# Optimization experiments

Hardware: AMD Instinct MI355X
Metric: run time of the kernel (lower is better)

## Reference

```python
import jax, jax.numpy as jnp
import numpy as np

M = 8      # bits // 8 experts
SUB = 8    # sub-code width per expert
HID = 256  # expert output classes (2**SUB)
BITS = 64
NCLS = 100
NUM_FLIP = (BITS // 32) ** 2  # 4


def _bit_flip(x, template, key):
    # torch: rand.argsort(-1) -> shuffledTemplate = template[idx]; x[mask] *= -1
    rand = jax.random.uniform(key, x.shape)
    idx = jnp.argsort(rand, axis=-1)
    mask = template[idx]
    return jnp.where(mask, -x, x)


def _map_net(x, W1, b1, W2, b2):
    # m independent Linear(8,256)->SiLU->Linear(256,256) experts over contiguous chunks
    N = x.shape[0]
    xs = x.reshape(N, M, SUB)
    h = jax.nn.silu(jnp.einsum('nmi,mih->nmh', xs, W1) + b1)
    return jnp.einsum('nmh,mho->nmo', h, W2) + b2  # [N, M, HID]


def setup_inputs() -> dict:
    key = jax.random.key(0)
    ks = jax.random.split(key, 10)
    N = 32768
    x = jax.random.normal(ks[0], (N, BITS), jnp.float32)
    # multi-label targets, guarantee >=1 positive per row (meanWeight divides by row sum)
    y = (jax.random.uniform(ks[1], (N, NCLS)) < 0.1).astype(jnp.int32)
    lab = jax.random.randint(ks[2], (N,), 0, NCLS)
    y = y.at[jnp.arange(N), lab].set(1)
    centroids = (jax.random.uniform(ks[3], (NCLS, BITS)) > 0.5).astype(jnp.float32)
    permIdx = jax.random.permutation(ks[4], BITS)

    def make_template(k):
        t = jnp.zeros(BITS, bool).at[:NUM_FLIP].set(True)
        return jax.random.permutation(k, t)

    template_map = make_template(ks[5])
    template_raw = make_template(ks[6])
    W1 = jax.random.normal(ks[7], (M, SUB, HID), jnp.float32) / np.sqrt(SUB)
    b1 = jnp.zeros((M, HID), jnp.float32)
    W2 = jax.random.normal(ks[8], (M, HID, HID), jnp.float32) / np.sqrt(HID)
    b2 = jnp.zeros((M, HID), jnp.float32)
    return dict(x=x, y=y, centroids=centroids, permIdx=permIdx,
                template_map=template_map, template_raw=template_raw,
                W1=W1, b1=b1, W2=W2, b2=b2)


def reference(x, y, centroids, permIdx, template_map, template_raw, W1, b1, W2, b2):
    N = x.shape[0]
    multiplier = 2 ** jnp.arange(SUB)  # [8]
    kmap, kraw = jax.random.split(jax.random.key(1))

    xp = x[:, permIdx]  # permuted codes [N, BITS]
    x_det = jax.lax.stop_gradient(xp)

    # ---- mapLoss path (x detached; mapper params still trained; dropout in eval) ----
    logits_map = _map_net(_bit_flip(x_det, template_map, kmap), W1, b1, W2, b2)  # [N,M,HID]
    raw_flipped = _bit_flip(x_det, template_raw, kraw)
    binary = raw_flipped.reshape(N, M, SUB) > 0
    target = (binary * multiplier).sum(-1)  # [N, M] decimal sub-codes
    lse = jax.nn.logsumexp(logits_map, axis=-1)
    picked = jnp.take_along_axis(logits_map, target[..., None], axis=-1)[..., 0]
    mapLoss = (lse - picked).mean(0).sum()  # sum over m of per-chunk CE means
    hitRate = (logits_map.argmax(-1) == target).astype(jnp.float32).mean()

    # ---- netLoss path (mapper on non-detached x, no flip; centers detached) ----
    hashCenter = jax.lax.stop_gradient(centroids[:, permIdx])  # [C, BITS]
    centerBits = hashCenter > 0
    centerTarget = (centerBits.reshape(NCLS, M, SUB) * multiplier).sum(-1)  # [C, M]
    logits_net = _map_net(xp, W1, b1, W2, b2)  # [N, M, HID]
    lse2 = jax.nn.logsumexp(logits_net, axis=-1)  # [N, M]
    # picked2[n,m,c] = logits_net[n, m, centerTarget[c, m]]
    picked2 = logits_net[:, jnp.arange(M)[:, None], centerTarget.T]  # [N, M, C]
    ce = lse2[..., None] - picked2  # [N, M, C]
    mask = y > 0
    w = mask.astype(jnp.float32)
    w = w / w.sum(-1, keepdims=True)  # meanWeight (mask * meanWeight == meanWeight)
    netLoss = (ce * w[:, None, :]).sum() / N

    # ---- codes-to-center Hamming distance, masked mean over (n, c) with y>0 ----
    xb = (xp > 0).astype(jnp.float32)
    cb = centerBits.astype(jnp.float32)
    ham = xb.sum(-1, keepdims=True) + cb.sum(-1)[None, :] - 2.0 * (xb @ cb.T)  # [N, C]
    mf = mask.astype(jnp.float32)
    codesToCenterDistance = (ham * mf).sum() / mf.sum()

    total = netLoss + mapLoss
    return (total, netLoss, mapLoss, hitRate, codesToCenterDistance)
```

## Files before the change

kernel.cpp:

```cpp
#include <hip/hip_runtime.h>
#include <stdint.h>

#define NR 32768
#define MM 8
#define NCLS 100
#define HALFN 1048576u
#define HSS 260
#define LGS 260
#define PSS 12

#define LOG2E 1.4426950408889634f
#define LN2F  0.6931471805599453f

typedef _Float16 h8 __attribute__((ext_vector_type(8)));
typedef _Float16 h4 __attribute__((ext_vector_type(4)));
typedef float f4 __attribute__((ext_vector_type(4)));
typedef unsigned long long ull;

__host__ __device__ inline void tf2x32(uint32_t k0, uint32_t k1, uint32_t x0, uint32_t x1,
                                       uint32_t& o0, uint32_t& o1) {
  uint32_t ks0 = k0, ks1 = k1, ks2 = k0 ^ k1 ^ 0x1BD11BDAu;
  x0 += ks0; x1 += ks1;
#define TFR(r) { x0 += x1; x1 = (x1 << r) | (x1 >> (32 - r)); x1 ^= x0; }
  TFR(13) TFR(15) TFR(26) TFR(6)  x0 += ks1; x1 += ks2 + 1u;
  TFR(17) TFR(29) TFR(16) TFR(24) x0 += ks2; x1 += ks0 + 2u;
  TFR(13) TFR(15) TFR(26) TFR(6)  x0 += ks0; x1 += ks1 + 3u;
  TFR(17) TFR(29) TFR(16) TFR(24) x0 += ks1; x1 += ks2 + 4u;
  TFR(13) TFR(15) TFR(26) TFR(6)  x0 += ks2; x1 += ks0 + 5u;
#undef TFR
  o0 = x0; o1 = x1;
}

__device__ inline int load_tmpl(const void* p, int lane) {
  const unsigned* pi = (const unsigned*)p;
  unsigned w = pi[lane];
  ull okF = __ballot(w == 0u || w == 0x3F800000u);
  ull onF = __ballot(w == 0x3F800000u);
  ull okI = __ballot(w <= 1u);
  ull onI = __ballot(w == 1u);
  if (okF == ~0ull && __popcll(onF) == 4) return (w == 0x3F800000u) ? 1 : 0;
  if (okI == ~0ull && __popcll(onI) == 4) return (int)w;
  const unsigned char* pb = (const unsigned char*)p;
  return pb[lane] ? 1 : 0;
}

__device__ inline uint32_t packh2(float a, float b) {
  union { _Float16 h[2]; uint32_t u; } cv;
  cv.h[0] = (_Float16)a; cv.h[1] = (_Float16)b;
  return cv.u;
}

__device__ inline ull flip_mask(ull tmask, uint32_t key) {
  ull fm = 0;
  while (tmask) {
    int p = __ffsll((long long)tmask) - 1;
    tmask &= tmask - 1;
    uint32_t kp = (uint32_t)__builtin_amdgcn_readlane((int)key, p);
    fm |= 1ull << __popcll(__ballot(key < kp));
  }
  return fm;
}

__global__ __launch_bounds__(256) void stage1p(
    const float* __restrict__ x, const int* __restrict__ y, const int* __restrict__ perm,
    const void* tmap, const void* traw,
    uint32_t km0, uint32_t km1, uint32_t kr0, uint32_t kr1,
    const float* __restrict__ W2, const float* __restrict__ W1,
    const float* __restrict__ B1, const float* __restrict__ B2,
    const float* __restrict__ centroids,
    _Float16* __restrict__ Wp, _Float16* __restrict__ Wp1, float* __restrict__ B2s,
    ull* __restrict__ cb64,
    uint32_t* __restrict__ xp16, uint32_t* __restrict__ xm16,
    ull* __restrict__ targ, ull* __restrict__ xb,
    float* __restrict__ winv, unsigned char* __restrict__ poslist, int* __restrict__ nposA) {
  int b = blockIdx.x, tid = threadIdx.x;
  if (b >= NR / 4) {
    int pb = b - NR / 4;
    if (pb < 256) {
      int gid = pb * 256 + tid;
      int lane6 = gid & 63, frag = gid >> 6;
      int NT = frag & 15, kt = (frag >> 4) & 7, m = frag >> 7;
      int q = lane6 >> 4, lr = lane6 & 15;
      const float* src = W2 + (size_t)m * 65536 + (size_t)(kt * 32 + q * 8) * 256 + NT * 16 + lr;
      h8 v;
#pragma unroll
      for (int j = 0; j < 8; j++) v[j] = (_Float16)src[j * 256];
      *(h8*)(Wp + (size_t)gid * 8) = v;
    } else if (pb < 288) {
      int idx = (pb - 256) * 256 + tid;
      int lane = idx & 63, t = (idx >> 6) & 15, m = idx >> 10;
      int q = lane >> 4, lr = lane & 15;
      h8 v;
#pragma unroll
      for (int j = 0; j < 8; j++) {
        float val = 0.0f;
        if (q == 0) val = W1[(size_t)(m * 8 + j) * 256 + t * 16 + lr] * LOG2E;
        else if (q == 1 && j == 0) val = B1[m * 256 + t * 16 + lr] * LOG2E;
        v[j] = (_Float16)val;
      }
      *(h8*)(Wp1 + (size_t)idx * 8) = v;
    } else if (pb < 313) {
      int c = (pb - 288) * 4 + (tid >> 6);
      int lane = tid & 63;
      ull bits = __ballot(centroids[c * 64 + perm[lane]] > 0.0f);
      if (lane == 0 && c < NCLS) cb64[c] = bits;
    } else {
#pragma unroll
      for (int j = 0; j < 8; j++) B2s[tid * 8 + j] = B2[tid * 8 + j] * LOG2E;
    }
    return;
  }

  __shared__ uint32_t ex[8][64];
  int wv = tid >> 6, lane = tid & 63;
  int odd = wv & 1, hi = wv >> 1;
  int n = b * 2 + odd + hi * 16384;

  int tm = load_tmpl(tmap, lane);
  int tr = load_tmpl(traw, lane);
  float xpv = x[n * 64 + perm[lane]];

  {
    uint32_t ic = (uint32_t)((b * 2 + hi) * 64 + lane);
    uint32_t k0 = odd ? kr0 : km0, k1 = odd ? kr1 : km1;
    uint32_t o0, o1;
    tf2x32(k0, k1, ic, ic + HALFN, o0, o1);
    ex[hi * 4 + odd * 2 + 0][lane] = o0;
    ex[hi * 4 + odd * 2 + 1][lane] = o1;
  }
  __syncthreads();
  uint32_t bm = ex[odd * 4 + 0 * 2 + hi][lane];
  uint32_t br = ex[odd * 4 + 1 * 2 + hi][lane];

  uint32_t kmk = ((bm >> 9) << 6) | (uint32_t)lane;
  uint32_t krk = ((br >> 9) << 6) | (uint32_t)lane;
  ull fm = flip_mask(__ballot(tm != 0), kmk);
  ull fr = flip_mask(__ballot(tr != 0), krk);
  int flipm = (int)((fm >> lane) & 1ull);
  int flipr = (int)((fr >> lane) & 1ull);

  float xmv = flipm ? -xpv : xpv;
  float rfv = flipr ? -xpv : xpv;
  float xp_o = __shfl_xor(xpv, 1);
  float xm_o = __shfl_xor(xmv, 1);
  if ((lane & 1) == 0) {
    xp16[n * 32 + (lane >> 1)] = packh2(xpv, xp_o);
    xm16[n * 32 + (lane >> 1)] = packh2(xmv, xm_o);
  }
  ull t64 = __ballot(rfv > 0.0f);
  ull b64v = __ballot(xpv > 0.0f);

  int c1 = y[(size_t)n * NCLS + lane] > 0;
  int c2 = (lane < NCLS - 64) ? (y[(size_t)n * NCLS + 64 + lane] > 0) : 0;
  ull p0 = __ballot(c1);
  ull p1 = __ballot(c2);
  int cnt0 = __popcll(p0);
  float cnt = (float)(cnt0 + __popcll(p1));

  unsigned char* pl = poslist + (size_t)n * 64;
  ull below = (lane == 0) ? 0ull : (~0ull >> (64 - lane));
  if (c1) pl[__popcll(p0 & below)] = (unsigned char)lane;
  if (c2) pl[cnt0 + __popcll(p1 & below)] = (unsigned char)(64 + lane);

  if (lane == 0) {
    targ[n] = t64;
    xb[n] = b64v;
    winv[n] = 1.0f / cnt;
    nposA[n] = cnt0 + __popcll(p1);
  }
}

__global__ __launch_bounds__(512, 8) void mapnet8(
    const uint32_t* __restrict__ Xm16, const uint32_t* __restrict__ Xp16,
    const _Float16* __restrict__ Wp1, const _Float16* __restrict__ Wp,
    const float* __restrict__ B2s,
    const ull* __restrict__ targ, const float* __restrict__ winv,
    const unsigned char* __restrict__ poslist, const int* __restrict__ nposA,
    const ull* __restrict__ cb64, const ull* __restrict__ xb,
    float* __restrict__ accbuf) {
  __shared__ union {
    _Float16 h[64 * HSS];
    float lg[32 * LGS];
  } u;
  __shared__ float ps[64 * PSS];
  __shared__ float pm[64 * PSS];
  __shared__ float sl[3];
  const int tid = threadIdx.x, lane = tid & 63, wv = tid >> 6;
  const int q = lane >> 4, lr = lane & 15;
  const int m = blockIdx.y, pass = blockIdx.z;
  const int n0 = blockIdx.x * 64;
  if (tid < 3) sl[tid] = 0.0f;

  if (pass == 2) {
    __syncthreads();
    int flat = blockIdx.y * 512 + blockIdx.x;
    int n = flat * 8 + wv;
    ull xv = xb[n];
    float px = (float)__popcll(xv);
    int np = nposA[n];
    float hs = 0.0f;
    if (lane < np) {
      int c = poslist[(size_t)n * 64 + lane];
      ull cb = cb64[c];
      hs = px + (float)__popcll(cb) - 2.0f * (float)__popcll(xv & cb);
    }
#pragma unroll
    for (int off = 1; off < 64; off <<= 1) hs += __shfl_xor(hs, off);
    if (lane == 0) {
      atomicAdd(&sl[0], hs);
      atomicAdd(&sl[1], (float)np);
    }
    __syncthreads();
    if (tid == 0) {
      float* slot = accbuf + (flat & 127) * 8;
      atomicAdd(&slot[3], sl[0]);
      atomicAdd(&slot[4], sl[1]);
    }
    return;
  }

  const uint32_t* Xin = pass ? Xp16 : Xm16;

  const int rb = wv & 3, tbase = (wv >> 2) * 8;
  h8 af;
  {
    const _Float16* xsrc = (const _Float16*)(Xin + (size_t)(n0 + rb * 16 + lr) * 32) + m * 8;
    h8 xv = *(const h8*)xsrc;
    h8 zero = {(_Float16)0.0f, (_Float16)0.0f, (_Float16)0.0f, (_Float16)0.0f,
               (_Float16)0.0f, (_Float16)0.0f, (_Float16)0.0f, (_Float16)0.0f};
    af = (q == 0) ? xv : zero;
    if (q == 1) af[0] = (_Float16)1.0f;
  }
#pragma unroll 4
  for (int tt = 0; tt < 8; tt++) {
    int t = tbase + tt;
    h8 wfrag = *(const h8*)(Wp1 + ((size_t)(m * 16 + t) * 64 + lane) * 8);
    f4 z = __builtin_amdgcn_mfma_f32_16x16x32_f16(wfrag, af, (f4){0.f, 0.f, 0.f, 0.f}, 0, 0, 0);
    h4 pk;
#pragma unroll
    for (int reg = 0; reg < 4; reg++) {
      float z2 = z[reg];
      pk[reg] = (_Float16)(z2 * __builtin_amdgcn_rcpf(1.0f + __builtin_amdgcn_exp2f(-z2)));
    }
    *(h4*)(u.h + (size_t)(rb * 16 + lr) * HSS + t * 16 + q * 4) = pk;
  }
  __syncthreads();

  f4 acc4[4][2];
  {
    f4 bv0 = *(const f4*)(B2s + m * 256 + wv * 32 + q * 4);
    f4 bv1 = *(const f4*)(B2s + m * 256 + wv * 32 + 16 + q * 4);
#pragma unroll
    for (int rt = 0; rt < 4; rt++) { acc4[rt][0] = bv0; acc4[rt][1] = bv1; }
  }
  const size_t wbase = (size_t)m * 65536;
#pragma unroll 2
  for (int kt = 0; kt < 8; kt++) {
    h8 bh0 = *(const h8*)(Wp + wbase + (((size_t)kt * 16 + wv * 2 + 0) * 64 + lane) * 8);
    h8 bh1 = *(const h8*)(Wp + wbase + (((size_t)kt * 16 + wv * 2 + 1) * 64 + lane) * 8);
#pragma unroll
    for (int rt = 0; rt < 4; rt++) {
      const _Float16* p = u.h + (rt * 16 + lr) * HSS + kt * 32 + q * 8;
      h4 lo = *(const h4*)p;
      h4 hi = *(const h4*)(p + 4);
      h8 ah = __builtin_shufflevector(lo, hi, 0, 1, 2, 3, 4, 5, 6, 7);
      acc4[rt][0] = __builtin_amdgcn_mfma_f32_16x16x32_f16(bh0, ah, acc4[rt][0], 0, 0, 0);
      acc4[rt][1] = __builtin_amdgcn_mfma_f32_16x16x32_f16(bh1, ah, acc4[rt][1], 0, 0, 0);
    }
  }

  float rsum[4], rmax[4];
#pragma unroll
  for (int rt = 0; rt < 4; rt++) {
    f4 l0 = acc4[rt][0], l1 = acc4[rt][1];
    float s = 0.0f;
#pragma unroll
    for (int reg = 0; reg < 4; reg++)
      s += __builtin_amdgcn_exp2f(l0[reg]) + __builtin_amdgcn_exp2f(l1[reg]);
    rsum[rt] = s;
    if (pass == 0) {
      float mv = fmaxf(l0[0], l1[0]);
#pragma unroll
      for (int reg = 1; reg < 4; reg++) mv = fmaxf(mv, fmaxf(l0[reg], l1[reg]));
      rmax[rt] = mv;
    }
  }
#pragma unroll
  for (int rt = 0; rt < 4; rt++) {
    rsum[rt] += __shfl_xor(rsum[rt], 16);
    rsum[rt] += __shfl_xor(rsum[rt], 32);
  }
  if (pass == 0) {
#pragma unroll
    for (int rt = 0; rt < 4; rt++) {
      rmax[rt] = fmaxf(rmax[rt], __shfl_xor(rmax[rt], 16));
      rmax[rt] = fmaxf(rmax[rt], __shfl_xor(rmax[rt], 32));
    }
  }
  if (lane < 16) {
#pragma unroll
    for (int rt = 0; rt < 4; rt++) {
      ps[(rt * 16 + lane) * PSS + wv] = rsum[rt];
      if (pass == 0) pm[(rt * 16 + lane) * PSS + wv] = rmax[rt];
    }
  }

  float partLoss = 0.0f, partHit = 0.0f;
  for (int ph = 0; ph < 2; ph++) {
    __syncthreads();
#pragma unroll
    for (int rt2 = 0; rt2 < 2; rt2++) {
#pragma unroll
      for (int nt = 0; nt < 2; nt++)
        *(f4*)&u.lg[(rt2 * 16 + lr) * LGS + wv * 32 + nt * 16 + q * 4] = acc4[ph * 2 + rt2][nt];
    }
    __syncthreads();
    int rl = tid >> 4;
    int grow = ph * 32 + rl;
    int n = n0 + grow;
    int cl = tid & 15;
    const float* lrow = u.lg + rl * LGS;
    if (pass == 0) {
      if (cl == 0) {
        f4 s0 = *(const f4*)(ps + grow * PSS);
        f4 s1 = *(const f4*)(ps + grow * PSS + 4);
        f4 ss = s0 + s1;
        float s = (ss[0] + ss[1]) + (ss[2] + ss[3]);
        f4 m0 = *(const f4*)(pm + grow * PSS);
        f4 m1 = *(const f4*)(pm + grow * PSS + 4);
        float mv = fmaxf(fmaxf(fmaxf(m0[0], m0[1]), fmaxf(m0[2], m0[3])),
                         fmaxf(fmaxf(m1[0], m1[1]), fmaxf(m1[2], m1[3])));
        int t = (int)((targ[n] >> (m * 8)) & 0xFFull);
        float pk = lrow[t];
        partLoss += __builtin_amdgcn_logf(s) - pk;
        partHit += (pk == mv) ? 1.0f : 0.0f;
      }
    } else {
      int np = nposA[n];
      const unsigned char* pl = poslist + (size_t)n * 64;
      float sp = 0.0f;
      for (int j2 = cl; j2 < np; j2 += 16) {
        int c = pl[j2];
        int t = (int)((cb64[c] >> (m * 8)) & 0xFFull);
        sp += lrow[t];
      }
#pragma unroll
      for (int off = 1; off < 16; off <<= 1) sp += __shfl_xor(sp, off);
      if (cl == 0) {
        f4 s0 = *(const f4*)(ps + grow * PSS);
        f4 s1 = *(const f4*)(ps + grow * PSS + 4);
        f4 ss = s0 + s1;
        float s = (ss[0] + ss[1]) + (ss[2] + ss[3]);
        partLoss += __builtin_amdgcn_logf(s) - winv[n] * sp;
      }
    }
  }
  partLoss += __shfl_xor(partLoss, 16); partHit += __shfl_xor(partHit, 16);
  partLoss += __shfl_xor(partLoss, 32); partHit += __shfl_xor(partHit, 32);
  if (lane == 0) {
    if (pass == 0) {
      atomicAdd(&sl[0], partLoss);
      atomicAdd(&sl[2], partHit);
    } else {
      atomicAdd(&sl[1], partLoss);
    }
  }
  __syncthreads();
  if (tid == 0) {
    float* slot = accbuf + (blockIdx.x & 127) * 8;
    if (pass == 0) {
      atomicAdd(&slot[0], sl[0]);
      atomicAdd(&slot[2], sl[2]);
    } else {
      atomicAdd(&slot[1], sl[1]);
    }
  }
}

__global__ __launch_bounds__(128) void finalk(const float* __restrict__ accbuf, float* __restrict__ out) {
  int t = threadIdx.x;
  float v0 = accbuf[t * 8 + 0], v1 = accbuf[t * 8 + 1], v2 = accbuf[t * 8 + 2];
  float v3 = accbuf[t * 8 + 3], v4 = accbuf[t * 8 + 4];
#pragma unroll
  for (int off = 1; off < 64; off <<= 1) {
    v0 += __shfl_xor(v0, off); v1 += __shfl_xor(v1, off); v2 += __shfl_xor(v2, off);
    v3 += __shfl_xor(v3, off); v4 += __shfl_xor(v4, off);
  }
  __shared__ float s[2][5];
  if ((t & 63) == 0) {
    s[t >> 6][0] = v0; s[t >> 6][1] = v1; s[t >> 6][2] = v2; s[t >> 6][3] = v3; s[t >> 6][4] = v4;
  }
  __syncthreads();
  if (t == 0) {
    float a0 = s[0][0] + s[1][0], a1 = s[0][1] + s[1][1], a2 = s[0][2] + s[1][2];
    float a3 = s[0][3] + s[1][3], a4 = s[0][4] + s[1][4];
    float netLoss = a1 * LN2F / (float)NR;
    float mapLoss = a0 * LN2F / (float)NR;
    out[0] = netLoss + mapLoss;
    out[1] = netLoss;
    out[2] = mapLoss;
    out[3] = a2 / (float)(NR * MM);
    out[4] = a3 / a4;
  }
}

extern "C" void kernel_launch(void* const* d_in, const int* in_sizes, int n_in,
                              void* d_out, int out_size, void* d_ws, size_t ws_size,
                              hipStream_t stream) {
  const float* x = (const float*)d_in[0];
  const int* y = (const int*)d_in[1];
  const float* centroids = (const float*)d_in[2];
  const int* perm = (const int*)d_in[3];
  const void* tmap = d_in[4];
  const void* traw = d_in[5];
  const float* W1 = (const float*)d_in[6];
  const float* B1 = (const float*)d_in[7];
  const float* W2 = (const float*)d_in[8];
  const float* B2 = (const float*)d_in[9];
  float* out = (float*)d_out;

  char* w = (char*)d_ws;
  float* accbuf = (float*)w;
  uint32_t* xp16 = (uint32_t*)(w + 4096);
  uint32_t* xm16 = xp16 + (size_t)NR * 32;
  ull* targ = (ull*)(xm16 + (size_t)NR * 32);
  ull* cb64 = targ + NR;
  ull* xb = cb64 + 128;
  float* winv = (float*)(xb + NR);
  int* nposA = (int*)(winv + NR);
  unsigned char* poslist = (unsigned char*)(nposA + NR);
  _Float16* Wp = (_Float16*)(poslist + (size_t)NR * 64);
  _Float16* Wp1 = Wp + (1 << 19);
  float* B2s = (float*)(Wp1 + (1 << 16));

  hipMemsetAsync(accbuf, 0, 4096, stream);

  uint32_t a0, b0, a1, b1;
  tf2x32(0u, 1u, 0u, 2u, a0, b0);
  tf2x32(0u, 1u, 1u, 3u, a1, b1);

  stage1p<<<NR / 4 + 314, 256, 0, stream>>>(x, y, perm, tmap, traw, a0, a1, b0, b1,
                                            W2, W1, B1, B2, centroids, Wp, Wp1, B2s, cb64,
                                            xp16, xm16, targ, xb, winv, poslist, nposA);
  dim3 g(NR / 64, MM, 3);
  mapnet8<<<g, 512, 0, stream>>>(xm16, xp16, Wp1, Wp, B2s, targ, winv, poslist, nposA,
                                 cb64, xb, accbuf);
  finalk<<<1, 128, 0, stream>>>(accbuf, out);
}
```

Measured before the change: 219.7 us.

## Process four rows per wave in prep kernel and pick targets from registers

The preprocessing kernel now has each wave handle four rows. It computes the threefry random words for both keys directly, so the shared-memory exchange and block barrier are gone, and it hoists the template ballots and perm load out of the per-row loop. In mapnet pass 0, the per-row target logit and hit test are read straight from the MFMA accumulators, using a small shared table of target indices and row maxima, instead of staging logits through shared memory twice. The LDS row stride changes from 260 to 264, which allows a single 16-byte h8 load for the A fragment. The cost is fewer blocks in stage1 and possible bank-conflict changes from the new stride.

```diff
diff --git a/kernel.cpp b/kernel.cpp
--- a/kernel.cpp
+++ b/kernel.cpp
@@ -5,8 +5,8 @@
 #define MM 8
 #define NCLS 100
 #define HALFN 1048576u
-#define HSS 260
-#define LGS 260
+#define HSS 264
+#define LGS 264
 #define PSS 12
 
 #define LOG2E 1.4426950408889634f
@@ -74,8 +74,8 @@
     ull* __restrict__ targ, ull* __restrict__ xb,
     float* __restrict__ winv, unsigned char* __restrict__ poslist, int* __restrict__ nposA) {
   int b = blockIdx.x, tid = threadIdx.x;
-  if (b >= NR / 4) {
-    int pb = b - NR / 4;
+  if (b >= 2048) {
+    int pb = b - 2048;
     if (pb < 256) {
       int gid = pb * 256 + tid;
       int lane6 = gid & 63, frag = gid >> 6;
@@ -111,62 +111,61 @@
     return;
   }
 
-  __shared__ uint32_t ex[8][64];
   int wv = tid >> 6, lane = tid & 63;
-  int odd = wv & 1, hi = wv >> 1;
-  int n = b * 2 + odd + hi * 16384;
-
   int tm = load_tmpl(tmap, lane);
   int tr = load_tmpl(traw, lane);
-  float xpv = x[n * 64 + perm[lane]];
-
+  ull tmm = __ballot(tm != 0);
+  ull trm = __ballot(tr != 0);
+  int pv = perm[lane];
+
+  int nbase = b * 8 + wv * 2;
+  uint32_t bmv[4], brv[4];
   {
-    uint32_t ic = (uint32_t)((b * 2 + hi) * 64 + lane);
-    uint32_t k0 = odd ? kr0 : km0, k1 = odd ? kr1 : km1;
-    uint32_t o0, o1;
-    tf2x32(k0, k1, ic, ic + HALFN, o0, o1);
-    ex[hi * 4 + odd * 2 + 0][lane] = o0;
-    ex[hi * 4 + odd * 2 + 1][lane] = o1;
-  }
-  __syncthreads();
-  uint32_t bm = ex[odd * 4 + 0 * 2 + hi][lane];
-  uint32_t br = ex[odd * 4 + 1 * 2 + hi][lane];
-
-  uint32_t kmk = ((bm >> 9) << 6) | (uint32_t)lane;
-  uint32_t krk = ((br >> 9) << 6) | (uint32_t)lane;
-  ull fm = flip_mask(__ballot(tm != 0), kmk);
-  ull fr = flip_mask(__ballot(tr != 0), krk);
-  int flipm = (int)((fm >> lane) & 1ull);
-  int flipr = (int)((fr >> lane) & 1ull);
-
-  float xmv = flipm ? -xpv : xpv;
-  float rfv = flipr ? -xpv : xpv;
-  float xp_o = __shfl_xor(xpv, 1);
-  float xm_o = __shfl_xor(xmv, 1);
-  if ((lane & 1) == 0) {
-    xp16[n * 32 + (lane >> 1)] = packh2(xpv, xp_o);
-    xm16[n * 32 + (lane >> 1)] = packh2(xmv, xm_o);
-  }
-  ull t64 = __ballot(rfv > 0.0f);
-  ull b64v = __ballot(xpv > 0.0f);
-
-  int c1 = y[(size_t)n * NCLS + lane] > 0;
-  int c2 = (lane < NCLS - 64) ? (y[(size_t)n * NCLS + 64 + lane] > 0) : 0;
-  ull p0 = __ballot(c1);
-  ull p1 = __ballot(c2);
-  int cnt0 = __popcll(p0);
-  float cnt = (float)(cnt0 + __popcll(p1));
-
-  unsigned char* pl = poslist + (size_t)n * 64;
-  ull below = (lane == 0) ? 0ull : (~0ull >> (64 - lane));
-  if (c1) pl[__popcll(p0 & below)] = (unsigned char)lane;
-  if (c2) pl[cnt0 + __popcll(p1 & below)] = (unsigned char)(64 + lane);
-
-  if (lane == 0) {
-    targ[n] = t64;
-    xb[n] = b64v;
-    winv[n] = 1.0f / cnt;
-    nposA[n] = cnt0 + __popcll(p1);
+    uint32_t iA = (uint32_t)(nbase * 64 + lane);
+    uint32_t iB = iA + 64u;
+    tf2x32(km0, km1, iA, iA + HALFN, bmv[0], bmv[2]);
+    tf2x32(kr0, kr1, iA, iA + HALFN, brv[0], brv[2]);
+    tf2x32(km0, km1, iB, iB + HALFN, bmv[1], bmv[3]);
+    tf2x32(kr0, kr1, iB, iB + HALFN, brv[1], brv[3]);
+  }
+  const int nn[4] = {nbase, nbase + 1, nbase + 16384, nbase + 16385};
+#pragma unroll
+  for (int rr = 0; rr < 4; rr++) {
+    int n = nn[rr];
+    float xpv = x[(size_t)n * 64 + pv];
+    uint32_t kmk = ((bmv[rr] >> 9) << 6) | (uint32_t)lane;
+    uint32_t krk = ((brv[rr] >> 9) << 6) | (uint32_t)lane;
+    ull fm = flip_mask(tmm, kmk);
+    ull fr = flip_mask(trm, krk);
+    float xmv = ((fm >> lane) & 1ull) ? -xpv : xpv;
+    float rfv = ((fr >> lane) & 1ull) ? -xpv : xpv;
+    float xp_o = __shfl_xor(xpv, 1);
+    float xm_o = __shfl_xor(xmv, 1);
+    if ((lane & 1) == 0) {
+      xp16[n * 32 + (lane >> 1)] = packh2(xpv, xp_o);
+      xm16[n * 32 + (lane >> 1)] = packh2(xmv, xm_o);
+    }
+    ull t64 = __ballot(rfv > 0.0f);
+    ull b64v = __ballot(xpv > 0.0f);
+
+    int c1 = y[(size_t)n * NCLS + lane] > 0;
+    int c2 = (lane < NCLS - 64) ? (y[(size_t)n * NCLS + 64 + lane] > 0) : 0;
+    ull p0 = __ballot(c1);
+    ull p1 = __ballot(c2);
+    int cnt0 = __popcll(p0);
+    float cnt = (float)(cnt0 + __popcll(p1));
+
+    unsigned char* pl = poslist + (size_t)n * 64;
+    ull below = (lane == 0) ? 0ull : (~0ull >> (64 - lane));
+    if (c1) pl[__popcll(p0 & below)] = (unsigned char)lane;
+    if (c2) pl[cnt0 + __popcll(p1 & below)] = (unsigned char)(64 + lane);
+
+    if (lane == 0) {
+      targ[n] = t64;
+      xb[n] = b64v;
+      winv[n] = 1.0f / cnt;
+      nposA[n] = cnt0 + __popcll(p1);
+    }
   }
 }
 
@@ -184,6 +183,8 @@
   } u;
   __shared__ float ps[64 * PSS];
   __shared__ float pm[64 * PSS];
+  __shared__ float mvA[64];
+  __shared__ int   tA[64];
   __shared__ float sl[3];
   const int tid = threadIdx.x, lane = tid & 63, wv = tid >> 6;
   const int q = lane >> 4, lr = lane & 15;
@@ -260,10 +261,7 @@
     h8 bh1 = *(const h8*)(Wp + wbase + (((size_t)kt * 16 + wv * 2 + 1) * 64 + lane) * 8);
 #pragma unroll
     for (int rt = 0; rt < 4; rt++) {
-      const _Float16* p = u.h + (rt * 16 + lr) * HSS + kt * 32 + q * 8;
-      h4 lo = *(const h4*)p;
-      h4 hi = *(const h4*)(p + 4);
-      h8 ah = __builtin_shufflevector(lo, hi, 0, 1, 2, 3, 4, 5, 6, 7);
+      h8 ah = *(const h8*)(u.h + (size_t)(rt * 16 + lr) * HSS + kt * 32 + q * 8);
       acc4[rt][0] = __builtin_amdgcn_mfma_f32_16x16x32_f16(bh0, ah, acc4[rt][0], 0, 0, 0);
       acc4[rt][1] = __builtin_amdgcn_mfma_f32_16x16x32_f16(bh1, ah, acc4[rt][1], 0, 0, 0);
     }
@@ -305,37 +303,70 @@
     }
   }
 
-  float partLoss = 0.0f, partHit = 0.0f;
-  for (int ph = 0; ph < 2; ph++) {
+  if (pass == 0) {
     __syncthreads();
-#pragma unroll
-    for (int rt2 = 0; rt2 < 2; rt2++) {
-#pragma unroll
-      for (int nt = 0; nt < 2; nt++)
-        *(f4*)&u.lg[(rt2 * 16 + lr) * LGS + wv * 32 + nt * 16 + q * 4] = acc4[ph * 2 + rt2][nt];
+    float myLse = 0.0f;
+    if (tid < 64) {
+      int row = tid, n = n0 + row;
+      f4 s0 = *(const f4*)(ps + row * PSS);
+      f4 s1 = *(const f4*)(ps + row * PSS + 4);
+      f4 ss = s0 + s1;
+      float s = (ss[0] + ss[1]) + (ss[2] + ss[3]);
+      f4 m0 = *(const f4*)(pm + row * PSS);
+      f4 m1 = *(const f4*)(pm + row * PSS + 4);
+      float mv = fmaxf(fmaxf(fmaxf(m0[0], m0[1]), fmaxf(m0[2], m0[3])),
+                       fmaxf(fmaxf(m1[0], m1[1]), fmaxf(m1[2], m1[3])));
+      mvA[row] = mv;
+      tA[row] = (int)((targ[n] >> (m * 8)) & 0xFFull);
+      myLse = __builtin_amdgcn_logf(s);
     }
     __syncthreads();
-    int rl = tid >> 4;
-    int grow = ph * 32 + rl;
-    int n = n0 + grow;
-    int cl = tid & 15;
-    const float* lrow = u.lg + rl * LGS;
-    if (pass == 0) {
-      if (cl == 0) {
-        f4 s0 = *(const f4*)(ps + grow * PSS);
-        f4 s1 = *(const f4*)(ps + grow * PSS + 4);
-        f4 ss = s0 + s1;
-        float s = (ss[0] + ss[1]) + (ss[2] + ss[3]);
-        f4 m0 = *(const f4*)(pm + grow * PSS);
-        f4 m1 = *(const f4*)(pm + grow * PSS + 4);
-        float mv = fmaxf(fmaxf(fmaxf(m0[0], m0[1]), fmaxf(m0[2], m0[3])),
-                         fmaxf(fmaxf(m1[0], m1[1]), fmaxf(m1[2], m1[3])));
-        int t = (int)((targ[n] >> (m * 8)) & 0xFFull);
-        float pk = lrow[t];
-        partLoss += __builtin_amdgcn_logf(s) - pk;
-        partHit += (pk == mv) ? 1.0f : 0.0f;
+    float pick = 0.0f, hit = 0.0f;
+    const int cbase = wv * 32 + q * 4;
+#pragma unroll
+    for (int rt = 0; rt < 4; rt++) {
+      int row = rt * 16 + lr;
+      int d0 = tA[row] - cbase;
+#pragma unroll
+      for (int nt = 0; nt < 2; nt++) {
+        int d = d0 - nt * 16;
+        if ((unsigned)d < 4u) {
+          f4 f = acc4[rt][nt];
+          float v = f[0];
+          v = (d == 1) ? f[1] : v;
+          v = (d == 2) ? f[2] : v;
+          v = (d == 3) ? f[3] : v;
+          pick += v;
+          hit += (v == mvA[row]) ? 1.0f : 0.0f;
+        }
       }
-    } else {
+    }
+    float lossC = myLse - pick;
+#pragma unroll
+    for (int off = 1; off < 64; off <<= 1) {
+      lossC += __shfl_xor(lossC, off);
+      hit += __shfl_xor(hit, off);
+    }
+    if (lane == 0) {
+      atomicAdd(&sl[0], lossC);
+      atomicAdd(&sl[2], hit);
+    }
+  } else {
+    float partLoss = 0.0f;
+    for (int ph = 0; ph < 2; ph++) {
+      __syncthreads();
+#pragma unroll
+      for (int rt2 = 0; rt2 < 2; rt2++) {
+#pragma unroll
+        for (int nt = 0; nt < 2; nt++)
+          *(f4*)&u.lg[(rt2 * 16 + lr) * LGS + wv * 32 + nt * 16 + q * 4] = acc4[ph * 2 + rt2][nt];
+      }
+      __syncthreads();
+      int rl = tid >> 4;
+      int grow = ph * 32 + rl;
+      int n = n0 + grow;
+      int cl = tid & 15;
+      const float* lrow = u.lg + rl * LGS;
       int np = nposA[n];
       const unsigned char* pl = poslist + (size_t)n * 64;
       float sp = 0.0f;
@@ -354,17 +385,11 @@
         partLoss += __builtin_amdgcn_logf(s) - winv[n] * sp;
       }
     }
-  }
-  partLoss += __shfl_xor(partLoss, 16); partHit += __shfl_xor(partHit, 16);
-  partLoss += __shfl_xor(partLoss, 32); partHit += __shfl_xor(partHit, 32);
-  if (lane == 0) {
-    if (pass == 0) {
-      atomicAdd(&sl[0], partLoss);
-      atomicAdd(&sl[2], partHit);
-    } else {
-      atomicAdd(&sl[1], partLoss);
-    }
-  }
+    partLoss += __shfl_xor(partLoss, 16);
+    partLoss += __shfl_xor(partLoss, 32);
+    if (lane == 0) atomicAdd(&sl[1], partLoss);
+  }
+
   __syncthreads();
   if (tid == 0) {
     float* slot = accbuf + (blockIdx.x & 127) * 8;
@@ -439,9 +464,9 @@
   tf2x32(0u, 1u, 0u, 2u, a0, b0);
   tf2x32(0u, 1u, 1u, 3u, a1, b1);
 
-  stage1p<<<NR / 4 + 314, 256, 0, stream>>>(x, y, perm, tmap, traw, a0, a1, b0, b1,
-                                            W2, W1, B1, B2, centroids, Wp, Wp1, B2s, cb64,
-                                            xp16, xm16, targ, xb, winv, poslist, nposA);
+  stage1p<<<2048 + 314, 256, 0, stream>>>(x, y, perm, tmap, traw, a0, a1, b0, b1,
+                                          W2, W1, B1, B2, centroids, Wp, Wp1, B2s, cb64,
+                                          xp16, xm16, targ, xb, winv, poslist, nposA);
   dim3 g(NR / 64, MM, 3);
   mapnet8<<<g, 512, 0, stream>>>(xm16, xp16, Wp1, Wp, B2s, targ, winv, poslist, nposA,
                                  cb64, xb, accbuf);
```

Result: slower. 263.1 us (+19.8%).
